# Kernel tuning notes

Measured on AMD Instinct MI355X. Metric: run time of the kernel, lower is better.

The kernel has to match this reference:

```python
import jax, jax.numpy as jnp
import numpy as np

BATCH_SIZE = 131072
N_NODES = 18  # per-graph nodes; N_NODES * c_out == 18 (input_size of fl1)
N_LAYERS = 2


def setup_inputs() -> dict:
    key = jax.random.key(0)
    ks = jax.random.split(key, 10)
    return {
        "node_features": jax.random.normal(ks[0], (BATCH_SIZE, N_NODES, 1), jnp.float32),
        "adj_matrix": jax.random.uniform(ks[1], (BATCH_SIZE, N_NODES, N_NODES), jnp.float32),
        "proj_w": jax.random.normal(ks[2], (1, 1), jnp.float32),
        "proj_b": jax.random.normal(ks[3], (1,), jnp.float32),
        "fl1_w": jax.random.normal(ks[4], (10, 18), jnp.float32) * 0.1,
        "fl1_b": jax.random.normal(ks[5], (10,), jnp.float32) * 0.1,
        "fl2_w": jax.random.normal(ks[6], (8, 10), jnp.float32) * 0.1,
        "fl2_b": jax.random.normal(ks[7], (8,), jnp.float32) * 0.1,
        "fl3_w": jax.random.normal(ks[8], (2, 8), jnp.float32) * 0.1,
        "fl3_b": jax.random.normal(ks[9], (2,), jnp.float32) * 0.1,
    }


def reference(node_features, adj_matrix, proj_w, proj_b, fl1_w, fl1_b, fl2_w, fl2_b, fl3_w, fl3_b):
    # GCN stack (original runs this under torch.no_grad())
    deg = adj_matrix.sum(axis=-1, keepdims=True)  # [B, N, 1]
    x = node_features
    for _ in range(N_LAYERS):
        h = x @ proj_w.T + proj_b           # [B, N, c_out]
        h = jnp.einsum('bnm,bmc->bnc', adj_matrix, h)
        h = h / deg
        x = jax.nn.relu(h)
    x = x.reshape(BATCH_SIZE, 18)
    # vectorized replacement of the per-element NaN-scrub Python loop
    x = jnp.where(jnp.isnan(x), jnp.float32(0.0), x)
    # small MLP head
    x = jax.nn.relu(x @ fl1_w.T + fl1_b)
    x = jax.nn.relu(x @ fl2_w.T + fl2_b)
    return x @ fl3_w.T + fl3_b
```

## Files before the change

kernel.cpp:

```cpp
#include <hip/hip_runtime.h>

#define NNODE  18
#define ADJ_B  1296
#define ADJ_F  324
#define TILE   40
#define TILE_BYTES (TILE * ADJ_B)
#define ROUNDS 13

__device__ __forceinline__ void gload_lds16(const void* g, void* l) {
    __builtin_amdgcn_global_load_lds((const __attribute__((address_space(1))) void*)g,
                                     (__attribute__((address_space(3))) void*)l, 16, 0, 0);
}

#define QB(v, P) __int_as_float(__builtin_amdgcn_ds_swizzle(__float_as_int(v), 0x8000 + 0x55 * (P)))
#define GATHER18(dst, src)                                                      \
    dst[0]=QB(src[0],0);  dst[1]=QB(src[0],1);  dst[2]=QB(src[0],2);  dst[3]=QB(src[0],3);   \
    dst[4]=QB(src[1],0);  dst[5]=QB(src[1],1);  dst[6]=QB(src[1],2);  dst[7]=QB(src[1],3);   \
    dst[8]=QB(src[2],0);  dst[9]=QB(src[2],1);  dst[10]=QB(src[2],2); dst[11]=QB(src[2],3);  \
    dst[12]=QB(src[3],0); dst[13]=QB(src[3],1); dst[14]=QB(src[3],2); dst[15]=QB(src[3],3);  \
    dst[16]=QB(src[4],0); dst[17]=QB(src[4],1);

__global__ __launch_bounds__(256, 3) void gcnn_fused(
    const float* __restrict__ nf,
    const float* __restrict__ adj,
    const float* __restrict__ proj_w, const float* __restrict__ proj_b,
    const float* __restrict__ w1, const float* __restrict__ b1,
    const float* __restrict__ w2, const float* __restrict__ b2,
    const float* __restrict__ w3, const float* __restrict__ b3,
    float* __restrict__ out,
    int B)
{
    extern __shared__ __align__(16) char smem[];
    const int tid  = threadIdx.x;
    const int wave = tid >> 6;
    const int lane = tid & 63;
    const int p    = tid & 3;
    const int Q    = tid >> 2;
    const int b0   = blockIdx.x * TILE;
    const int nb   = min(TILE, B - b0);
    const int nbytes = nb * ADJ_B;
    const int b    = b0 + Q;

    float x[NNODE];
    if (Q < nb) {
        const float2* __restrict__ xp = (const float2*)(nf + (size_t)b * NNODE);
        #pragma unroll
        for (int j = 0; j < 9; ++j) { float2 v = xp[j]; x[2*j] = v.x; x[2*j+1] = v.y; }
    }

    const char* __restrict__ gbase = (const char*)adj + (size_t)b0 * ADJ_B;
    #pragma unroll
    for (int r = 0; r < ROUNDS; ++r) {
        const int ow  = r * 4096 + wave * 1024;
        const int off = ow + lane * 16;
        if (off < nbytes) gload_lds16(gbase + off, smem + ow);
    }
    __syncthreads();

    if (Q < nb) {
        float a[5][NNODE];
        const float* __restrict__ my = (const float*)smem + Q * ADJ_F;
        #pragma unroll
        for (int t = 0; t < 5; ++t) {
            int r  = 4 * t + p;
            int ro = r < NNODE ? r : NNODE - 1;
            const float2* __restrict__ rp = (const float2*)(my + ro * NNODE);
            #pragma unroll
            for (int j = 0; j < 9; ++j) { float2 v = rp[j]; a[t][2*j] = v.x; a[t][2*j+1] = v.y; }
        }

        const float pw = proj_w[0], pb = proj_b[0];

        float inv[5], h[5];
        #pragma unroll
        for (int t = 0; t < 5; ++t) {
            float d = 0.f, s = 0.f;
            #pragma unroll
            for (int m = 0; m < NNODE; ++m) { d += a[t][m]; s += a[t][m] * x[m]; }
            inv[t] = 1.0f / d;
            h[t]   = fmaxf(0.f, pw * s * inv[t] + pb);
        }

        float hf[NNODE];
        GATHER18(hf, h)

        float y[5];
        #pragma unroll
        for (int t = 0; t < 5; ++t) {
            float s = 0.f;
            #pragma unroll
            for (int m = 0; m < NNODE; ++m) s += a[t][m] * hf[m];
            float v = fmaxf(0.f, pw * s * inv[t] + pb);
            y[t] = (v != v) ? 0.f : v;
        }

        float yf[NNODE];
        GATHER18(yf, y)

        float z1[10];
        #pragma unroll
        for (int k = 0; k < 10; ++k) {
            float s = b1[k];
            #pragma unroll
            for (int j = 0; j < NNODE; ++j) s += w1[k*NNODE + j] * yf[j];
            z1[k] = fmaxf(0.f, s);
        }
        float z2[8];
        #pragma unroll
        for (int k = 0; k < 8; ++k) {
            float s = b2[k];
            #pragma unroll
            for (int j = 0; j < 10; ++j) s += w2[k*10 + j] * z1[j];
            z2[k] = fmaxf(0.f, s);
        }
        float o0 = b3[0], o1 = b3[1];
        #pragma unroll
        for (int j = 0; j < 8; ++j) { o0 += w3[j] * z2[j]; o1 += w3[8 + j] * z2[j]; }

        if (p == 0)
            *(float2*)(out + (size_t)b * 2) = make_float2(o0, o1);
    }
}

extern "C" void kernel_launch(void* const* d_in, const int* in_sizes, int n_in,
                              void* d_out, int out_size, void* d_ws, size_t ws_size,
                              hipStream_t stream) {
    const float* nf  = (const float*)d_in[0];
    const float* adj = (const float*)d_in[1];
    const float* pw  = (const float*)d_in[2];
    const float* pb  = (const float*)d_in[3];
    const float* w1  = (const float*)d_in[4];
    const float* b1  = (const float*)d_in[5];
    const float* w2  = (const float*)d_in[6];
    const float* b2  = (const float*)d_in[7];
    const float* w3  = (const float*)d_in[8];
    const float* b3  = (const float*)d_in[9];
    float* out = (float*)d_out;

    const int B = in_sizes[0] / NNODE;
    const int grid = (B + TILE - 1) / TILE;

    hipFuncSetAttribute(reinterpret_cast<const void*>(gcnn_fused),
                        hipFuncAttributeMaxDynamicSharedMemorySize, TILE_BYTES);

    gcnn_fused<<<grid, 256, TILE_BYTES, stream>>>(nf, adj, pw, pb, w1, b1, w2, b2, w3, b3, out, B);
}
```

Before: 35.79 us.

## Make kernel persistent with double-buffered LDS prefetch of adjacency tiles

Result: slower. 50.64 us (+41.5%).

```diff
diff --git a/kernel.cpp b/kernel.cpp
--- a/kernel.cpp
+++ b/kernel.cpp
@@ -3,9 +3,11 @@
 #define NNODE  18
 #define ADJ_B  1296
 #define ADJ_F  324
-#define TILE   40
-#define TILE_BYTES (TILE * ADJ_B)
-#define ROUNDS 13
+#define TILE   20
+#define BUF_B  (TILE * ADJ_B)
+#define WSTRIPE (BUF_B / 4)
+#define SOPS   7
+#define GRID   768
 
 __device__ __forceinline__ void gload_lds16(const void* g, void* l) {
     __builtin_amdgcn_global_load_lds((const __attribute__((address_space(1))) void*)g,
@@ -21,104 +23,127 @@
     dst[16]=QB(src[4],0); dst[17]=QB(src[4],1);
 
 __global__ __launch_bounds__(256, 3) void gcnn_fused(
-    const float* __restrict__ nf,
-    const float* __restrict__ adj,
+    const float* __restrict__ nf, const float* __restrict__ adj,
     const float* __restrict__ proj_w, const float* __restrict__ proj_b,
     const float* __restrict__ w1, const float* __restrict__ b1,
     const float* __restrict__ w2, const float* __restrict__ b2,
     const float* __restrict__ w3, const float* __restrict__ b3,
-    float* __restrict__ out,
-    int B)
+    float* __restrict__ out, int B)
 {
     extern __shared__ __align__(16) char smem[];
     const int tid  = threadIdx.x;
     const int wave = tid >> 6;
     const int lane = tid & 63;
-    const int p    = tid & 3;
-    const int Q    = tid >> 2;
-    const int b0   = blockIdx.x * TILE;
-    const int nb   = min(TILE, B - b0);
-    const int nbytes = nb * ADJ_B;
-    const int b    = b0 + Q;
+    const int p    = lane & 3;
+    const int q    = lane >> 2;
+    const int bt   = wave * 5 + q;
+    const int NT   = (B + TILE - 1) / TILE;
+    const unsigned adjLim = (unsigned)B * ADJ_B - 16;
 
-    float x[NNODE];
-    if (Q < nb) {
-        const float2* __restrict__ xp = (const float2*)(nf + (size_t)b * NNODE);
+    char* bA = smem;
+    char* bB = smem + BUF_B;
+
+    auto stage = [&](int t, char* buf) {
+        const unsigned base = (unsigned)t * BUF_B + (unsigned)(wave * WSTRIPE) + lane * 16;
+        char* ldst = buf + wave * WSTRIPE;
         #pragma unroll
-        for (int j = 0; j < 9; ++j) { float2 v = xp[j]; x[2*j] = v.x; x[2*j+1] = v.y; }
-    }
+        for (int c = 0; c < 6; ++c)
+            gload_lds16((const char*)adj + min(base + c * 1024u, adjLim), ldst + c * 1024);
+        if (lane < 21)
+            gload_lds16((const char*)adj + min(base + 6144u, adjLim), ldst + 6144);
+    };
 
-    const char* __restrict__ gbase = (const char*)adj + (size_t)b0 * ADJ_B;
-    #pragma unroll
-    for (int r = 0; r < ROUNDS; ++r) {
-        const int ow  = r * 4096 + wave * 1024;
-        const int off = ow + lane * 16;
-        if (off < nbytes) gload_lds16(gbase + off, smem + ow);
-    }
-    __syncthreads();
+    int t = blockIdx.x;
+    stage(t, bA);
 
-    if (Q < nb) {
-        float a[5][NNODE];
-        const float* __restrict__ my = (const float*)smem + Q * ADJ_F;
-        #pragma unroll
-        for (int t = 0; t < 5; ++t) {
-            int r  = 4 * t + p;
-            int ro = r < NNODE ? r : NNODE - 1;
-            const float2* __restrict__ rp = (const float2*)(my + ro * NNODE);
+    for (; t < NT; t += GRID) {
+        const int b = t * TILE + bt;
+        const bool act = (q < 5) && (b < B);
+
+        float x[NNODE];
+        if (act) {
+            const float2* __restrict__ xp = (const float2*)(nf + (size_t)b * NNODE);
             #pragma unroll
-            for (int j = 0; j < 9; ++j) { float2 v = rp[j]; a[t][2*j] = v.x; a[t][2*j+1] = v.y; }
+            for (int j = 0; j < 9; ++j) { float2 v = xp[j]; x[2*j] = v.x; x[2*j+1] = v.y; }
+        }
+        asm volatile("" ::: "memory");
+
+        const int tn = t + GRID;
+        if (tn < NT) {
+            stage(tn, bB);
+            asm volatile("s_waitcnt vmcnt(7)" ::: "memory");
+        } else {
+            asm volatile("s_waitcnt vmcnt(0)" ::: "memory");
+        }
+        __builtin_amdgcn_s_barrier();
+
+        if (act) {
+            float a[5][NNODE];
+            const float* __restrict__ my = (const float*)bA + bt * ADJ_F;
+            #pragma unroll
+            for (int u = 0; u < 5; ++u) {
+                int r  = 4 * u + p;
+                int ro = r < NNODE ? r : NNODE - 1;
+                const float2* __restrict__ rp = (const float2*)(my + ro * NNODE);
+                #pragma unroll
+                for (int j = 0; j < 9; ++j) { float2 v = rp[j]; a[u][2*j] = v.x; a[u][2*j+1] = v.y; }
+            }
+
+            const float pw = proj_w[0], pb = proj_b[0];
+
+            float inv[5], h[5];
+            #pragma unroll
+            for (int u = 0; u < 5; ++u) {
+                float d = 0.f, s = 0.f;
+                #pragma unroll
+                for (int m = 0; m < NNODE; ++m) { d += a[u][m]; s += a[u][m] * x[m]; }
+                inv[u] = 1.0f / d;
+                h[u]   = fmaxf(0.f, pw * s * inv[u] + pb);
+            }
+
+            float hf[NNODE];
+            GATHER18(hf, h)
+
+            float y[5];
+            #pragma unroll
+            for (int u = 0; u < 5; ++u) {
+                float s = 0.f;
+                #pragma unroll
+                for (int m = 0; m < NNODE; ++m) s += a[u][m] * hf[m];
+                float v = fmaxf(0.f, pw * s * inv[u] + pb);
+                y[u] = (v != v) ? 0.f : v;
+            }
+
+            float yf[NNODE];
+            GATHER18(yf, y)
+
+            float z1[10];
+            #pragma unroll
+            for (int k = 0; k < 10; ++k) {
+                float s = b1[k];
+                #pragma unroll
+                for (int j = 0; j < NNODE; ++j) s += w1[k*NNODE + j] * yf[j];
+                z1[k] = fmaxf(0.f, s);
+            }
+            float z2[8];
+            #pragma unroll
+            for (int k = 0; k < 8; ++k) {
+                float s = b2[k];
+                #pragma unroll
+                for (int j = 0; j < 10; ++j) s += w2[k*10 + j] * z1[j];
+                z2[k] = fmaxf(0.f, s);
+            }
+            float o0 = b3[0], o1 = b3[1];
+            #pragma unroll
+            for (int j = 0; j < 8; ++j) { o0 += w3[j] * z2[j]; o1 += w3[8 + j] * z2[j]; }
+
+            if (p == 0)
+                *(float2*)(out + (size_t)b * 2) = make_float2(o0, o1);
         }
 
-        const float pw = proj_w[0], pb = proj_b[0];
-
-        float inv[5], h[5];
-        #pragma unroll
-        for (int t = 0; t < 5; ++t) {
-            float d = 0.f, s = 0.f;
-            #pragma unroll
-            for (int m = 0; m < NNODE; ++m) { d += a[t][m]; s += a[t][m] * x[m]; }
-            inv[t] = 1.0f / d;
-            h[t]   = fmaxf(0.f, pw * s * inv[t] + pb);
-        }
-
-        float hf[NNODE];
-        GATHER18(hf, h)
-
-        float y[5];
-        #pragma unroll
-        for (int t = 0; t < 5; ++t) {
-            float s = 0.f;
-            #pragma unroll
-            for (int m = 0; m < NNODE; ++m) s += a[t][m] * hf[m];
-            float v = fmaxf(0.f, pw * s * inv[t] + pb);
-            y[t] = (v != v) ? 0.f : v;
-        }
-
-        float yf[NNODE];
-        GATHER18(yf, y)
-
-        float z1[10];
-        #pragma unroll
-        for (int k = 0; k < 10; ++k) {
-            float s = b1[k];
-            #pragma unroll
-            for (int j = 0; j < NNODE; ++j) s += w1[k*NNODE + j] * yf[j];
-            z1[k] = fmaxf(0.f, s);
-        }
-        float z2[8];
-        #pragma unroll
-        for (int k = 0; k < 8; ++k) {
-            float s = b2[k];
-            #pragma unroll
-            for (int j = 0; j < 10; ++j) s += w2[k*10 + j] * z1[j];
-            z2[k] = fmaxf(0.f, s);
-        }
-        float o0 = b3[0], o1 = b3[1];
-        #pragma unroll
-        for (int j = 0; j < 8; ++j) { o0 += w3[j] * z2[j]; o1 += w3[8 + j] * z2[j]; }
-
-        if (p == 0)
-            *(float2*)(out + (size_t)b * 2) = make_float2(o0, o1);
+        asm volatile("" ::: "memory");
+        __builtin_amdgcn_s_barrier();
+        char* tmp = bA; bA = bB; bB = tmp;
     }
 }
 
@@ -138,10 +163,10 @@
     float* out = (float*)d_out;
 
     const int B = in_sizes[0] / NNODE;
-    const int grid = (B + TILE - 1) / TILE;
+    const size_t ldsBytes = 2 * BUF_B;
 
     hipFuncSetAttribute(reinterpret_cast<const void*>(gcnn_fused),
-                        hipFuncAttributeMaxDynamicSharedMemorySize, TILE_BYTES);
+                        hipFuncAttributeMaxDynamicSharedMemorySize, (int)ldsBytes);
 
-    gcnn_fused<<<grid, 256, TILE_BYTES, stream>>>(nf, adj, pw, pb, w1, b1, w2, b2, w3, b3, out, B);
+    gcnn_fused<<<GRID, 256, ldsBytes, stream>>>(nf, adj, pw, pb, w1, b1, w2, b2, w3, b3, out, B);
 }
```
